# Kernel optimization log

Hardware: AMD Instinct MI355X
Metric: run time of the kernel (lower is better)

Reference implementation:

```python
import jax, jax.numpy as jnp
import numpy as np

N1, N2, B, D = 16000, 16000, 4096, 256


def setup_inputs() -> dict:
    key = jax.random.key(0)
    ks = jax.random.split(key, 11)
    inp = {
        "x1": jax.random.normal(ks[0], (N1, D), dtype=jnp.float32),
        "x_name1": jax.random.normal(ks[1], (N1, D), dtype=jnp.float32),
        "onehot1": jax.random.normal(ks[2], (N1, D), dtype=jnp.float32),
        "x2": jax.random.normal(ks[3], (N2, D), dtype=jnp.float32),
        "x_name2": jax.random.normal(ks[4], (N2, D), dtype=jnp.float32),
        "onehot2": jax.random.normal(ks[5], (N2, D), dtype=jnp.float32),
        # mk MLP params: Linear(D, D//2) -> ReLU -> Linear(D//2, 1) -> Sigmoid
        "W1": jax.random.normal(ks[6], (D, D // 2), dtype=jnp.float32) * 0.05,
        "b1": jnp.zeros((D // 2,), dtype=jnp.float32),
        "W2": jax.random.normal(ks[7], (D // 2, 1), dtype=jnp.float32) * 0.05,
        "b2": jnp.zeros((1,), dtype=jnp.float32),
        "data_batch": jnp.stack(
            [
                jax.random.randint(ks[8], (B,), 0, N1),
                jax.random.randint(ks[9], (B,), 0, N2),
            ],
            axis=1,
        ).astype(jnp.int64),
    }
    return inp


def _mk(h, W1, b1, W2, b2):
    # tiny 2-layer MLP gate with sigmoid output, h: [B, D] -> [B, 1]
    return jax.nn.sigmoid(jax.nn.relu(h @ W1 + b1) @ W2 + b2)


def _side(Xg, Xfull, W1, b1, W2, b2):
    # Xg: [3, B, D] gathered channels; Xfull: [3, N, D] full tables of the OTHER side
    # cross-attention: softmax(Xg @ Xfull^T) @ Xfull + residual
    A = jax.nn.softmax(jnp.einsum("cbd,cnd->cbn", Xg, Xfull), axis=-1)  # [3,B,N]
    Re = jnp.einsum("cbn,cnd->cbd", A, Xfull) + Xg  # [3,B,D]
    kg = jax.nn.softmax(
        jnp.concatenate(
            [_mk(Re[0], W1, b1, W2, b2), _mk(Re[1], W1, b1, W2, b2), _mk(Re[2], W1, b1, W2, b2)],
            axis=-1,
        ),
        axis=-1,
    )  # [B,3]
    return kg


def reference(x1, x_name1, onehot1, x2, x_name2, onehot2, W1, b1, W2, b2, data_batch):
    i1 = data_batch[:, 0]
    i2 = data_batch[:, 1]
    X1 = jnp.stack([x1[i1], x_name1[i1], onehot1[i1]])  # [3,B,D]
    X2 = jnp.stack([x2[i2], x_name2[i2], onehot2[i2]])  # [3,B,D]
    X1_full = jnp.stack([x2, x_name2, onehot2])  # [3,N2,D]
    X2_full = jnp.stack([x1, x_name1, onehot1])  # [3,N1,D]
    kg1 = _side(X1, X1_full, W1, b1, W2, b2)  # [B,3]
    kg2 = _side(X2, X2_full, W1, b1, W2, b2)  # [B,3]
    x_name1_out = x_name1.at[i1].set(x_name1[i1] * kg1[:, 1:2])
    onehot1_out = onehot1.at[i1].set(onehot1[i1] * kg1[:, 2:3])
    x_name2_out = x_name2.at[i2].set(x_name2[i2] * kg2[:, 1:2])
    onehot2_out = onehot2.at[i2].set(onehot2[i2] * kg2[:, 2:3])
    return (x1, x_name1_out, onehot1_out, x2, x_name2_out, onehot2_out)
```

## Files before the change

### kernel.cpp

```cpp
#include <hip/hip_runtime.h>
#include <math.h>

typedef _Float16 f16;
typedef _Float16 f16x4 __attribute__((ext_vector_type(4)));
typedef _Float16 f16x8 __attribute__((ext_vector_type(8)));
typedef float    f32x4 __attribute__((ext_vector_type(4)));

#define N_ROWS 16000
#define DIM    256
#define BATCH  4096
#define TK     64
#define NTILE  250
#define TPS    125
#define QT     64
#define LTP    72
#define VPAD   72

__device__ __forceinline__ void gload16(const void* g, void* l) {
  __builtin_amdgcn_global_load_lds(
      (const __attribute__((address_space(1))) void*)g,
      (__attribute__((address_space(3))) void*)l, 16, 0, 0);
}


__global__ __launch_bounds__(256) void k_pack(
    const float* __restrict__ m0, const float* __restrict__ m1, const float* __restrict__ m2,
    const float* __restrict__ m3, const float* __restrict__ m4, const float* __restrict__ m5,
    unsigned char* __restrict__ Kimg, unsigned char* __restrict__ Vimg)
{
  __shared__ f16 lt[64][LTP];
  const float* mats[6] = {m0, m1, m2, m3, m4, m5};
  int bid = blockIdx.x;
  int db  = bid & 3;
  int tn  = (bid >> 2) % NTILE;
  int me  = bid / (NTILE * 4);
  const float* src = mats[me];
  int tid = threadIdx.x;
  unsigned char* Kt = Kimg + ((size_t)(me * NTILE + tn) << 15);
  unsigned char* Vt = Vimg + ((size_t)(me * NTILE + tn) << 15);
#pragma unroll
  for (int i = 0; i < 4; ++i) {
    int cidx = i * 256 + tid;
    int r = cidx >> 4, cc = (cidx & 15) * 4;
    float4 f = *(const float4*)(src + (size_t)(tn * 64 + r) * DIM + db * 64 + cc);
    f16x4 h = {(f16)f.x, (f16)f.y, (f16)f.z, (f16)f.w};
    *(f16x4*)&lt[r][cc] = h;
    *(f16x4*)(Kt + r * 512 + ((db * 128 + cc * 2) ^ ((r & 7) << 4))) = h;
  }
  __syncthreads();
#pragma unroll
  for (int i = 0; i < 4; ++i) {
    int cidx = i * 256 + tid;
    int dl = cidx >> 4, nc4 = (cidx & 15) * 4;
    f16x4 hv = { lt[nc4 + 0][dl], lt[nc4 + 1][dl], lt[nc4 + 2][dl], lt[nc4 + 3][dl] };
    int d = db * 64 + dl;
    *(f16x4*)(Vt + d * 128 + ((nc4 * 2) ^ ((dl & 7) << 4))) = hv;
  }
}

__global__ __launch_bounds__(256) void k_gather(
    const float* __restrict__ m0, const float* __restrict__ m1, const float* __restrict__ m2,
    const float* __restrict__ m3, const float* __restrict__ m4, const float* __restrict__ m5,
    const int* __restrict__ batch, f16* __restrict__ Qg)
{
  const float* mats[6] = {m0, m1, m2, m3, m4, m5};
  int gid  = blockIdx.x * 4 + (threadIdx.x >> 6);
  int lane = threadIdx.x & 63;
  int s   = gid / (3 * BATCH);
  int rem = gid - s * 3 * BATCH;
  int c   = rem / BATCH;
  int b   = rem - c * BATCH;
  int idx = batch[(size_t)b * 2 + s];
  const float* src = mats[(s == 0 ? 0 : 3) + c] + (size_t)idx * DIM;
  float4 f = *(const float4*)(src + lane * 4);
  f16x4 h = {(f16)f.x, (f16)f.y, (f16)f.z, (f16)f.w};
  *(f16x4*)(Qg + (size_t)gid * DIM + lane * 4) = h;
}

__global__ __launch_bounds__(256, 2) void k_attn(
    const unsigned char* __restrict__ Kimg, const unsigned char* __restrict__ Vimg,
    const f16* __restrict__ Qg, f16* __restrict__ Onorm, float* __restrict__ ml)
{
  __shared__ unsigned char shK[32768];
  __shared__ unsigned char shV[32768];
  __shared__ f16 shP[4][16][VPAD];

  const int bid = blockIdx.x;
  const int v  = bid & 1;
  const int t  = (bid >> 1) & 63;
  const int cs = bid >> 7;
  const int s  = cs / 3, c = cs - s * 3;
  const int kvmat = (s == 0) ? (3 + c) : c;

  const int tid  = threadIdx.x;
  const int lane = tid & 63;
  const int w    = tid >> 6;
  const int l15  = lane & 15;
  const int quad = lane >> 4;
  const int xr   = (l15 & 7) << 4;

  const f16* Qrow = Qg + ((size_t)cs * BATCH + (size_t)t * QT + w * 16 + l15) * DIM + quad * 8;
  f16x8 qf[8];
#pragma unroll
  for (int kt = 0; kt < 8; ++kt) qf[kt] = *(const f16x8*)(Qrow + kt * 32);

  f32x4 O[16];
#pragma unroll
  for (int i = 0; i < 16; ++i) O[i] = (f32x4){0.f, 0.f, 0.f, 0.f};
  float m_r[4] = {-INFINITY, -INFINITY, -INFINITY, -INFINITY};
  float l_r[4] = {0.f, 0.f, 0.f, 0.f};

  const unsigned char* gK0 = Kimg + ((size_t)(kvmat * NTILE) << 15);
  const unsigned char* gV0 = Vimg + ((size_t)(kvmat * NTILE) << 15);
  const int o = tid * 16;

  for (int tile = v * TPS; tile < v * TPS + TPS; ++tile) {
    const unsigned char* gK = gK0 + ((size_t)tile << 15);
    const unsigned char* gV = gV0 + ((size_t)tile << 15);
#pragma unroll
    for (int i = 0; i < 8; ++i) gload16(gK + i * 4096 + o, shK + i * 4096 + o);
#pragma unroll
    for (int i = 0; i < 8; ++i) gload16(gV + i * 4096 + o, shV + i * 4096 + o);
    __syncthreads();

    f32x4 sacc[4];
#pragma unroll
    for (int nc = 0; nc < 4; ++nc) sacc[nc] = (f32x4){0.f, 0.f, 0.f, 0.f};
    __builtin_amdgcn_s_setprio(1);
#pragma unroll
    for (int kt = 0; kt < 8; ++kt) {
#pragma unroll
      for (int nc = 0; nc < 4; ++nc) {
        f16x8 kf = *(const f16x8*)(shK + (nc * 16 + l15) * 512 + ((kt * 64 + quad * 16) ^ xr));
        sacc[nc] = __builtin_amdgcn_mfma_f32_16x16x32_f16(qf[kt], kf, sacc[nc], 0, 0, 0);
      }
    }
    __builtin_amdgcn_s_setprio(0);

    float alpha[4];
    bool upd = false;
#pragma unroll
    for (int r = 0; r < 4; ++r) {
      float mx = fmaxf(fmaxf(sacc[0][r], sacc[1][r]), fmaxf(sacc[2][r], sacc[3][r]));
#pragma unroll
      for (int off = 1; off < 16; off <<= 1) mx = fmaxf(mx, __shfl_xor(mx, off, 64));
      float mnew = fmaxf(m_r[r], mx);
      alpha[r] = __expf(m_r[r] - mnew);
      upd = upd || (mnew > m_r[r]);
      m_r[r] = mnew;
    }
    float rowsum[4] = {0.f, 0.f, 0.f, 0.f};
#pragma unroll
    for (int nc = 0; nc < 4; ++nc) {
#pragma unroll
      for (int r = 0; r < 4; ++r) {
        float p = __expf(sacc[nc][r] - m_r[r]);
        rowsum[r] += p;
        shP[w][quad * 4 + r][nc * 16 + l15] = (f16)p;
      }
    }
#pragma unroll
    for (int r = 0; r < 4; ++r) {
#pragma unroll
      for (int off = 1; off < 16; off <<= 1) rowsum[r] += __shfl_xor(rowsum[r], off, 64);
      l_r[r] = l_r[r] * alpha[r] + rowsum[r];
    }
    if (__any(upd)) {
#pragma unroll
      for (int nc = 0; nc < 16; ++nc) {
#pragma unroll
        for (int r = 0; r < 4; ++r) O[nc][r] *= alpha[r];
      }
    }

    f16x8 pf0 = *(const f16x8*)&shP[w][l15][quad * 8];
    f16x8 pf1 = *(const f16x8*)&shP[w][l15][32 + quad * 8];
    __builtin_amdgcn_s_setprio(1);
#pragma unroll
    for (int nc = 0; nc < 16; ++nc) {
      f16x8 vf0 = *(const f16x8*)(shV + (nc * 16 + l15) * 128 + ((quad * 16) ^ xr));
      O[nc] = __builtin_amdgcn_mfma_f32_16x16x32_f16(pf0, vf0, O[nc], 0, 0, 0);
      f16x8 vf1 = *(const f16x8*)(shV + (nc * 16 + l15) * 128 + ((64 + quad * 16) ^ xr));
      O[nc] = __builtin_amdgcn_mfma_f32_16x16x32_f16(pf1, vf1, O[nc], 0, 0, 0);
    }
    __builtin_amdgcn_s_setprio(0);
    __syncthreads();
  }

  const size_t orow0 = (size_t)(v * 6 + cs) * BATCH + (size_t)t * QT + w * 16;
  if (l15 == 0) {
#pragma unroll
    for (int r = 0; r < 4; ++r) {
      size_t row = orow0 + quad * 4 + r;
      ml[row * 2 + 0] = m_r[r];
      ml[row * 2 + 1] = l_r[r];
    }
  }
#pragma unroll
  for (int r = 0; r < 4; ++r) {
    float inv = 1.0f / l_r[r];
    size_t row = orow0 + quad * 4 + r;
#pragma unroll
    for (int nc = 0; nc < 16; ++nc)
      Onorm[row * DIM + nc * 16 + l15] = (f16)(O[nc][r] * inv);
  }
}

__global__ __launch_bounds__(256, 2) void k_combine(
    const float* __restrict__ W1, const float* __restrict__ b1,
    const float* __restrict__ W2, const float* __restrict__ b2,
    const f16* __restrict__ Qg, const f16* __restrict__ Onorm,
    const float* __restrict__ ml, float* __restrict__ mval)
{
  __shared__ f16 w1s[DIM * 128];
  __shared__ float reb[4][DIM];
  __shared__ float w2s[128];
  __shared__ float b1s[128];
  int tid = threadIdx.x;
#pragma unroll
  for (int i = 0; i < 32; ++i) {
    int e = i * 1024 + tid * 4;
    float4 f = *(const float4*)(W1 + e);
    f16x4 h = {(f16)f.x, (f16)f.y, (f16)f.z, (f16)f.w};
    *(f16x4*)&w1s[e] = h;
  }
  if (tid < 128) { w2s[tid] = W2[tid]; b1s[tid] = b1[tid]; }
  float b2v = b2[0];
  __syncthreads();

  int w = tid >> 6, lane = tid & 63;
  for (int rr = 0; rr < 8; ++rr) {
    int grow = blockIdx.x * 32 + w * 8 + rr;
    float m0 = ml[grow * 2],            l0 = ml[grow * 2 + 1];
    float m1 = ml[(24576 + grow) * 2],  l1 = ml[(24576 + grow) * 2 + 1];
    float M  = fmaxf(m0, m1);
    float w0  = l0 * __expf(m0 - M);
    float w1v = l1 * __expf(m1 - M);
    float inv = 1.f / (w0 + w1v);
    w0 *= inv; w1v *= inv;
    f16x4 o0 = *(const f16x4*)(Onorm + (size_t)grow * DIM + lane * 4);
    f16x4 o1 = *(const f16x4*)(Onorm + (size_t)(24576 + grow) * DIM + lane * 4);
    f16x4 qv = *(const f16x4*)(Qg + (size_t)grow * DIM + lane * 4);
#pragma unroll
    for (int k = 0; k < 4; ++k)
      reb[w][lane * 4 + k] = w0 * (float)o0[k] + w1v * (float)o1[k] + (float)qv[k];
    float acc0 = b1s[lane], acc1 = b1s[lane + 64];
    for (int d = 0; d < DIM; ++d) {
      float rv = reb[w][d];
      acc0 += rv * (float)w1s[d * 128 + lane];
      acc1 += rv * (float)w1s[d * 128 + 64 + lane];
    }
    float part = fmaxf(acc0, 0.f) * w2s[lane] + fmaxf(acc1, 0.f) * w2s[lane + 64];
#pragma unroll
    for (int off = 1; off < 64; off <<= 1) part += __shfl_xor(part, off, 64);
    if (lane == 0) mval[grow] = 1.f / (1.f + __expf(-(part + b2v)));
  }
}

__global__ __launch_bounds__(256) void k_copy(
    const float* __restrict__ m0, const float* __restrict__ m1, const float* __restrict__ m2,
    const float* __restrict__ m3, const float* __restrict__ m4, const float* __restrict__ m5,
    float* __restrict__ out)
{
  const float* mats[6] = {m0, m1, m2, m3, m4, m5};
  int arr = blockIdx.x / 4000;
  int chunk = (blockIdx.x - arr * 4000) * 256 + threadIdx.x;
  float4 v = *(const float4*)(mats[arr] + (size_t)chunk * 4);
  *(float4*)(out + (size_t)arr * 4096000 + (size_t)chunk * 4) = v;
}

__global__ __launch_bounds__(256) void k_scatter(
    const float* __restrict__ m0, const float* __restrict__ m1, const float* __restrict__ m2,
    const float* __restrict__ m3, const float* __restrict__ m4, const float* __restrict__ m5,
    const int* __restrict__ batch, const float* __restrict__ mval,
    float* __restrict__ out)
{
  const float* mats[6] = {m0, m1, m2, m3, m4, m5};
  int gid  = blockIdx.x * 4 + (threadIdx.x >> 6);
  int lane = threadIdx.x & 63;
  int s = gid >> 12;
  int b = gid & 4095;
  int idx = batch[(size_t)b * 2 + s];
  float v0 = mval[(s * 3 + 0) * BATCH + b];
  float v1 = mval[(s * 3 + 1) * BATCH + b];
  float v2 = mval[(s * 3 + 2) * BATCH + b];
  float mx = fmaxf(v0, fmaxf(v1, v2));
  float e0 = __expf(v0 - mx), e1 = __expf(v1 - mx), e2 = __expf(v2 - mx);
  float inv = 1.f / (e0 + e1 + e2);
  float kgn = e1 * inv;
  float kgo = e2 * inv;
  int a1 = s * 3 + 1, a2 = s * 3 + 2;
  const float* s1 = mats[a1] + (size_t)idx * DIM;
  const float* s2 = mats[a2] + (size_t)idx * DIM;
  float4 f1 = *(const float4*)(s1 + lane * 4);
  float4 f2 = *(const float4*)(s2 + lane * 4);
  float4 r1 = {f1.x * kgn, f1.y * kgn, f1.z * kgn, f1.w * kgn};
  float4 r2 = {f2.x * kgo, f2.y * kgo, f2.z * kgo, f2.w * kgo};
  *(float4*)(out + (size_t)a1 * 4096000 + (size_t)idx * DIM + lane * 4) = r1;
  *(float4*)(out + (size_t)a2 * 4096000 + (size_t)idx * DIM + lane * 4) = r2;
}

extern "C" void kernel_launch(void* const* d_in, const int* in_sizes, int n_in,
                              void* d_out, int out_size, void* d_ws, size_t ws_size,
                              hipStream_t stream)
{
  const float* x1  = (const float*)d_in[0];
  const float* xn1 = (const float*)d_in[1];
  const float* oh1 = (const float*)d_in[2];
  const float* x2  = (const float*)d_in[3];
  const float* xn2 = (const float*)d_in[4];
  const float* oh2 = (const float*)d_in[5];
  const float* W1  = (const float*)d_in[6];
  const float* b1  = (const float*)d_in[7];
  const float* W2  = (const float*)d_in[8];
  const float* b2  = (const float*)d_in[9];
  const int*   batch = (const int*)d_in[10];
  float* out = (float*)d_out;

  unsigned char* Kimg = (unsigned char*)d_out;
  unsigned char* Vimg = (unsigned char*)d_out + 49152000;

  char* ws = (char*)d_ws;
  f16*   Qg    = (f16*)(ws);
  f16*   Onorm = (f16*)(ws + 12582912);
  float* ml    = (float*)(ws + 37748736);
  float* mval  = (float*)(ws + 38141952);

  k_pack   <<<6000, 256, 0, stream>>>(x1, xn1, oh1, x2, xn2, oh2, Kimg, Vimg);
  k_gather <<<6144, 256, 0, stream>>>(x1, xn1, oh1, x2, xn2, oh2, batch, Qg);
  k_attn   <<<768,  256, 0, stream>>>(Kimg, Vimg, Qg, Onorm, ml);
  k_combine<<<768,  256, 0, stream>>>(W1, b1, W2, b2, Qg, Onorm, ml, mval);
  k_copy   <<<24000, 256, 0, stream>>>(x1, xn1, oh1, x2, xn2, oh2, out);
  k_scatter<<<2048, 256, 0, stream>>>(x1, xn1, oh1, x2, xn2, oh2, batch, mval, out);
}
```

Baseline: 1.158 ms.

## Halve KV tile to 32 rows and raise attention occupancy to four blocks

The KV tile size drops from 64 to 32 rows, which halves the shared-memory K/V buffers, and the launch bound rises from 2 to 4 blocks per CU. The pack kernel is rewritten to emit 16KB tile images with a new interleaved, swizzled V layout, and the PV MFMA reads that layout with a single k=32 step. The aim is more resident waves to hide global-to-LDS load latency. In exchange there are twice as many tiles and barriers, the per-tile softmax and rescale overhead doubles relative to MFMA work, and the tighter register budget may cause spills.

```diff
diff --git a/kernel.cpp b/kernel.cpp
--- a/kernel.cpp
+++ b/kernel.cpp
@@ -8,13 +8,13 @@
 
 #define N_ROWS 16000
 #define DIM    256
+#define TK     32
+#define NTILE  500
+#define TPS    250
 #define BATCH  4096
-#define TK     64
-#define NTILE  250
-#define TPS    125
 #define QT     64
 #define LTP    72
-#define VPAD   72
+#define PPAD   40
 
 __device__ __forceinline__ void gload16(const void* g, void* l) {
   __builtin_amdgcn_global_load_lds(
@@ -32,12 +32,10 @@
   const float* mats[6] = {m0, m1, m2, m3, m4, m5};
   int bid = blockIdx.x;
   int db  = bid & 3;
-  int tn  = (bid >> 2) % NTILE;
-  int me  = bid / (NTILE * 4);
+  int tn  = (bid >> 2) % 250;
+  int me  = bid / (250 * 4);
   const float* src = mats[me];
   int tid = threadIdx.x;
-  unsigned char* Kt = Kimg + ((size_t)(me * NTILE + tn) << 15);
-  unsigned char* Vt = Vimg + ((size_t)(me * NTILE + tn) << 15);
 #pragma unroll
   for (int i = 0; i < 4; ++i) {
     int cidx = i * 256 + tid;
@@ -45,7 +43,8 @@
     float4 f = *(const float4*)(src + (size_t)(tn * 64 + r) * DIM + db * 64 + cc);
     f16x4 h = {(f16)f.x, (f16)f.y, (f16)f.z, (f16)f.w};
     *(f16x4*)&lt[r][cc] = h;
-    *(f16x4*)(Kt + r * 512 + ((db * 128 + cc * 2) ^ ((r & 7) << 4))) = h;
+    size_t g = (size_t)(me * NTILE + tn * 2 + (r >> 5)) << 14;
+    *(f16x4*)(Kimg + g + (r & 31) * 512 + (((db * 64 + cc) * 2) ^ ((r & 7) << 4))) = h;
   }
   __syncthreads();
 #pragma unroll
@@ -53,8 +52,11 @@
     int cidx = i * 256 + tid;
     int dl = cidx >> 4, nc4 = (cidx & 15) * 4;
     f16x4 hv = { lt[nc4 + 0][dl], lt[nc4 + 1][dl], lt[nc4 + 2][dl], lt[nc4 + 3][dl] };
-    int d = db * 64 + dl;
-    *(f16x4*)(Vt + d * 128 + ((nc4 * 2) ^ ((dl & 7) << 4))) = hv;
+    size_t g = (size_t)(me * NTILE + tn * 2 + (nc4 >> 5)) << 14;
+    int kvl = nc4 & 31;
+    int dp  = db * 32 + (dl >> 1);
+    int inner = (dl & 1) * 64 + kvl * 2;
+    *(f16x4*)(Vimg + g + dp * 128 + (inner ^ (((dl >> 1) & 7) << 4))) = hv;
   }
 }
 
@@ -77,13 +79,13 @@
   *(f16x4*)(Qg + (size_t)gid * DIM + lane * 4) = h;
 }
 
-__global__ __launch_bounds__(256, 2) void k_attn(
+__global__ __launch_bounds__(256, 4) void k_attn(
     const unsigned char* __restrict__ Kimg, const unsigned char* __restrict__ Vimg,
     const f16* __restrict__ Qg, f16* __restrict__ Onorm, float* __restrict__ ml)
 {
-  __shared__ unsigned char shK[32768];
-  __shared__ unsigned char shV[32768];
-  __shared__ f16 shP[4][16][VPAD];
+  __shared__ unsigned char shK[16384];
+  __shared__ unsigned char shV[16384];
+  __shared__ f16 shP[4][16][PPAD];
 
   const int bid = blockIdx.x;
   const int v  = bid & 1;
@@ -110,27 +112,27 @@
   float m_r[4] = {-INFINITY, -INFINITY, -INFINITY, -INFINITY};
   float l_r[4] = {0.f, 0.f, 0.f, 0.f};
 
-  const unsigned char* gK0 = Kimg + ((size_t)(kvmat * NTILE) << 15);
-  const unsigned char* gV0 = Vimg + ((size_t)(kvmat * NTILE) << 15);
+  const unsigned char* gK0 = Kimg + ((size_t)(kvmat * NTILE) << 14);
+  const unsigned char* gV0 = Vimg + ((size_t)(kvmat * NTILE) << 14);
   const int o = tid * 16;
 
   for (int tile = v * TPS; tile < v * TPS + TPS; ++tile) {
-    const unsigned char* gK = gK0 + ((size_t)tile << 15);
-    const unsigned char* gV = gV0 + ((size_t)tile << 15);
-#pragma unroll
-    for (int i = 0; i < 8; ++i) gload16(gK + i * 4096 + o, shK + i * 4096 + o);
-#pragma unroll
-    for (int i = 0; i < 8; ++i) gload16(gV + i * 4096 + o, shV + i * 4096 + o);
+    const unsigned char* gK = gK0 + ((size_t)tile << 14);
+    const unsigned char* gV = gV0 + ((size_t)tile << 14);
+#pragma unroll
+    for (int i = 0; i < 4; ++i) gload16(gK + i * 4096 + o, shK + i * 4096 + o);
+#pragma unroll
+    for (int i = 0; i < 4; ++i) gload16(gV + i * 4096 + o, shV + i * 4096 + o);
     __syncthreads();
 
-    f32x4 sacc[4];
-#pragma unroll
-    for (int nc = 0; nc < 4; ++nc) sacc[nc] = (f32x4){0.f, 0.f, 0.f, 0.f};
+    f32x4 sacc[2];
+#pragma unroll
+    for (int nc = 0; nc < 2; ++nc) sacc[nc] = (f32x4){0.f, 0.f, 0.f, 0.f};
     __builtin_amdgcn_s_setprio(1);
 #pragma unroll
     for (int kt = 0; kt < 8; ++kt) {
 #pragma unroll
-      for (int nc = 0; nc < 4; ++nc) {
+      for (int nc = 0; nc < 2; ++nc) {
         f16x8 kf = *(const f16x8*)(shK + (nc * 16 + l15) * 512 + ((kt * 64 + quad * 16) ^ xr));
         sacc[nc] = __builtin_amdgcn_mfma_f32_16x16x32_f16(qf[kt], kf, sacc[nc], 0, 0, 0);
       }
@@ -141,7 +143,7 @@
     bool upd = false;
 #pragma unroll
     for (int r = 0; r < 4; ++r) {
-      float mx = fmaxf(fmaxf(sacc[0][r], sacc[1][r]), fmaxf(sacc[2][r], sacc[3][r]));
+      float mx = fmaxf(sacc[0][r], sacc[1][r]);
 #pragma unroll
       for (int off = 1; off < 16; off <<= 1) mx = fmaxf(mx, __shfl_xor(mx, off, 64));
       float mnew = fmaxf(m_r[r], mx);
@@ -151,7 +153,7 @@
     }
     float rowsum[4] = {0.f, 0.f, 0.f, 0.f};
 #pragma unroll
-    for (int nc = 0; nc < 4; ++nc) {
+    for (int nc = 0; nc < 2; ++nc) {
 #pragma unroll
       for (int r = 0; r < 4; ++r) {
         float p = __expf(sacc[nc][r] - m_r[r]);
@@ -173,15 +175,13 @@
       }
     }
 
-    f16x8 pf0 = *(const f16x8*)&shP[w][l15][quad * 8];
-    f16x8 pf1 = *(const f16x8*)&shP[w][l15][32 + quad * 8];
+    f16x8 pf = *(const f16x8*)&shP[w][l15][quad * 8];
     __builtin_amdgcn_s_setprio(1);
 #pragma unroll
     for (int nc = 0; nc < 16; ++nc) {
-      f16x8 vf0 = *(const f16x8*)(shV + (nc * 16 + l15) * 128 + ((quad * 16) ^ xr));
-      O[nc] = __builtin_amdgcn_mfma_f32_16x16x32_f16(pf0, vf0, O[nc], 0, 0, 0);
-      f16x8 vf1 = *(const f16x8*)(shV + (nc * 16 + l15) * 128 + ((64 + quad * 16) ^ xr));
-      O[nc] = __builtin_amdgcn_mfma_f32_16x16x32_f16(pf1, vf1, O[nc], 0, 0, 0);
+      f16x8 vf = *(const f16x8*)(shV + (nc * 8 + (l15 >> 1)) * 128 +
+                                 (((l15 & 1) * 64 + quad * 16) ^ ((l15 >> 1) << 4)));
+      O[nc] = __builtin_amdgcn_mfma_f32_16x16x32_f16(pf, vf, O[nc], 0, 0, 0);
     }
     __builtin_amdgcn_s_setprio(0);
     __syncthreads();
```

Result: slower. 1.233 ms (+6.5%).
